# Kernel tuning notes

Measured on AMD Instinct MI355X. Metric: run time of the kernel, lower is better.

## Reference

```python
import jax, jax.numpy as jnp
import numpy as np

HEAD = 8


def setup_inputs() -> dict:
    key0 = jax.random.key(0)
    ks = jax.random.split(key0, 16)
    B, K, RD, NH = 16, 1024, 1024, 1024
    s = 0.02
    inp = {
        "v": jax.random.normal(ks[0], (B, K, RD), jnp.float32),
        "key": jax.random.normal(ks[1], (B, K, RD), jnp.float32),
        "query": jax.random.normal(ks[2], (B, K, RD), jnp.float32),
        "mask": jax.random.randint(ks[3], (B, 1, 1, K), 0, 2).astype(bool),
        # FCNet([relation_dim, num_hid], act='') == Linear(relation_dim, num_hid)
        "Wq": jax.random.normal(ks[4], (RD, NH), jnp.float32) * s,
        "bq": jnp.zeros((NH,), jnp.float32),
        "Wk": jax.random.normal(ks[5], (RD, NH), jnp.float32) * s,
        "bk": jnp.zeros((NH,), jnp.float32),
        "Wv": jax.random.normal(ks[6], (RD, NH), jnp.float32) * s,
        "bv": jnp.zeros((NH,), jnp.float32),
        "Wm": jax.random.normal(ks[7], (NH, NH), jnp.float32) * s,
        "bm": jnp.zeros((NH,), jnp.float32),
    }
    return inp


def reference(v, key, query, mask, Wq, bq, Wk, bk, Wv, bv, Wm, bm):
    B, K, _ = v.shape
    NH = Wq.shape[1]
    dk = NH // HEAD

    def split_heads(x):  # [B,K,NH] -> [B,H,K,dk]
        return x.reshape(B, K, HEAD, dk).transpose(0, 2, 1, 3)

    q = split_heads(query @ Wq + bq)
    k = split_heads(key @ Wk + bk)
    vv = split_heads(v @ Wv + bv)

    scores = jnp.einsum("bhqd,bhkd->bhqk", q, k) / jnp.sqrt(jnp.float32(dk))
    scores = jnp.where(mask, jnp.float32(-1e9), scores)
    att = jax.nn.softmax(scores, axis=-1)  # dropout is identity at eval
    atted = jnp.einsum("bhqk,bhkd->bhqd", att, vv)
    atted = atted.transpose(0, 2, 1, 3).reshape(B, K, NH)
    atted = atted @ Wm + bm
    return atted, att
```

## Files before the change

### kernel.cpp

```cpp
#include <hip/hip_runtime.h>

typedef unsigned short u16;
typedef __attribute__((ext_vector_type(8))) short short8;
typedef __attribute__((ext_vector_type(4))) float floatx4;

#define MFMA16(a, b, c) __builtin_amdgcn_mfma_f32_16x16x32_bf16(a, b, c, 0, 0, 0)

#define BB 16
#define KK 1024
#define NH 1024
#define HD 8
#define DK 128
#define ATT_OFF 16777216

typedef const __attribute__((address_space(1))) unsigned gl_u32;
typedef __attribute__((address_space(3))) unsigned lds_u32;

__device__ __forceinline__ u16 f2bf(float x) {
  unsigned u = __builtin_bit_cast(unsigned, x);
  u += 0x7fffu + ((u >> 16) & 1u);
  return (u16)(u >> 16);
}

__device__ __forceinline__ void gload16(const u16* g, u16* l) {
  __builtin_amdgcn_global_load_lds((gl_u32*)g, (lds_u32*)l, 16, 0, 0);
}

__global__ __launch_bounds__(256) void cast3_bf16x8(
    const float* __restrict__ i0, const float* __restrict__ i1,
    const float* __restrict__ i2, u16* __restrict__ o0, u16* __restrict__ o1,
    u16* __restrict__ o2) {
  const float* in = blockIdx.y == 0 ? i0 : (blockIdx.y == 1 ? i1 : i2);
  u16* out = blockIdx.y == 0 ? o0 : (blockIdx.y == 1 ? o1 : o2);
  const size_t i = ((size_t)blockIdx.x * 256 + threadIdx.x) * 8;
  float4 f0 = *(const float4*)(in + i);
  float4 f1 = *(const float4*)(in + i + 4);
  union { u16 u[8]; uint4 v; } p;
  p.u[0] = f2bf(f0.x); p.u[1] = f2bf(f0.y); p.u[2] = f2bf(f0.z); p.u[3] = f2bf(f0.w);
  p.u[4] = f2bf(f1.x); p.u[5] = f2bf(f1.y); p.u[6] = f2bf(f1.z); p.u[7] = f2bf(f1.w);
  *(uint4*)(out + i) = p.v;
}

__global__ __launch_bounds__(256) void tr_w(const float* __restrict__ in,
                                            u16* __restrict__ out) {
  __shared__ u16 t[32][36];
  const int tid = threadIdx.x;
  const int bx = blockIdx.x * 32;
  const int by = blockIdx.y * 32;
  const int r = tid >> 3, c4 = (tid & 7) * 4;
  float4 f = *(const float4*)(in + (size_t)(by + r) * 1024 + bx + c4);
  t[r][c4 + 0] = f2bf(f.x);
  t[r][c4 + 1] = f2bf(f.y);
  t[r][c4 + 2] = f2bf(f.z);
  t[r][c4 + 3] = f2bf(f.w);
  __syncthreads();
  union { u16 u[4]; uint2 v; } p;
#pragma unroll
  for (int i = 0; i < 4; i++) p.u[i] = t[c4 + i][r];
  *(uint2*)(out + (size_t)(bx + r) * 1024 + by + c4) = p.v;
}

__global__ __launch_bounds__(256) void tr_head(const u16* __restrict__ vvb,
                                               u16* __restrict__ vvT) {
  __shared__ u16 t[32][36];
  const int tid = threadIdx.x;
  const int bh = blockIdx.z, b = bh >> 3, h = bh & 7;
  const int i0 = blockIdx.x * 32, d0 = blockIdx.y * 32;
  const int r = tid >> 3, c4 = (tid & 7) * 4;
  union { u16 u[4]; uint2 v; } p;
  p.v = *(const uint2*)(vvb + (size_t)(b * KK + i0 + r) * NH + h * DK + d0 + c4);
  t[r][c4 + 0] = p.u[0];
  t[r][c4 + 1] = p.u[1];
  t[r][c4 + 2] = p.u[2];
  t[r][c4 + 3] = p.u[3];
  __syncthreads();
#pragma unroll
  for (int i = 0; i < 4; i++) p.u[i] = t[c4 + i][r];
  *(uint2*)(vvT + (size_t)(bh * DK + d0 + r) * KK + i0 + c4) = p.v;
}

__device__ __forceinline__ void gemm_body(
    const u16* __restrict__ Ab, const u16* __restrict__ Bb,
    const float* __restrict__ bias, u16* __restrict__ Cb, float* __restrict__ Cf,
    const int Kd, const int ldc, const int nBase, const int mBase) {
  __shared__ __align__(16) u16 As[2][128 * 32];
  __shared__ __align__(16) u16 Bs[2][128 * 32];
  const int tid = threadIdx.x;
  const int wid = tid >> 6, lane = tid & 63;
  const int wm = (wid & 1) * 64, wn = (wid >> 1) * 64;
  const int lm = lane & 15, lq = lane >> 4;
  const int rIn = lane >> 2;
  const int sSlot = (lane & 3) * 8;

  const u16* aS0 = Ab + (size_t)(mBase + (wid * 2 + 0) * 16 + rIn) * Kd + sSlot;
  const u16* aS1 = Ab + (size_t)(mBase + (wid * 2 + 1) * 16 + rIn) * Kd + sSlot;
  const u16* bS0 = Bb + (size_t)(nBase + (wid * 2 + 0) * 16 + rIn) * Kd + sSlot;
  const u16* bS1 = Bb + (size_t)(nBase + (wid * 2 + 1) * 16 + rIn) * Kd + sSlot;

  floatx4 acc[4][4] = {};

  gload16(aS0, &As[0][(wid * 2 + 0) * 512]);
  gload16(aS1, &As[0][(wid * 2 + 1) * 512]);
  gload16(bS0, &Bs[0][(wid * 2 + 0) * 512]);
  gload16(bS1, &Bs[0][(wid * 2 + 1) * 512]);
  __syncthreads();

  int cur = 0;
  for (int k0 = 0; k0 < Kd; k0 += 32) {
    const int nxt = cur ^ 1;
    if (k0 + 32 < Kd) {
      gload16(aS0 + k0 + 32, &As[nxt][(wid * 2 + 0) * 512]);
      gload16(aS1 + k0 + 32, &As[nxt][(wid * 2 + 1) * 512]);
      gload16(bS0 + k0 + 32, &Bs[nxt][(wid * 2 + 0) * 512]);
      gload16(bS1 + k0 + 32, &Bs[nxt][(wid * 2 + 1) * 512]);
    }
    short8 af[4], bfr[4];
#pragma unroll
    for (int t = 0; t < 4; t++) {
      af[t]  = *(const short8*)&As[cur][(wm + t * 16 + lm) * 32 + lq * 8];
      bfr[t] = *(const short8*)&Bs[cur][(wn + t * 16 + lm) * 32 + lq * 8];
    }
#pragma unroll
    for (int i = 0; i < 4; i++)
#pragma unroll
      for (int j = 0; j < 4; j++)
        acc[i][j] = MFMA16(af[i], bfr[j], acc[i][j]);
    __syncthreads();
    cur = nxt;
  }

#pragma unroll
  for (int i = 0; i < 4; i++) {
    const int rowL = wm + i * 16 + lq * 4;
#pragma unroll
    for (int j = 0; j < 4; j++) {
      const int col = nBase + wn + j * 16 + lm;
      const float bval = bias ? bias[col] : 0.0f;
      const size_t base = (size_t)(mBase + rowL) * ldc + col;
#pragma unroll
      for (int r = 0; r < 4; r++) {
        const float v = acc[i][j][r] + bval;
        if (Cb) Cb[base + (size_t)r * ldc] = f2bf(v);
        if (Cf) Cf[base + (size_t)r * ldc] = v;
      }
    }
  }
}

__device__ __forceinline__ int2 swz_grid() {
  const int flat = blockIdx.x + 8 * blockIdx.y;
  const int xcd = flat & 7, idx = flat >> 3;
  const int nflat = xcd * 128 + idx;
  return make_int2((nflat & 7) * 128, (nflat >> 3) * 128);
}

__global__ __launch_bounds__(256, 2) void gemm_bt(
    const u16* __restrict__ A, const u16* __restrict__ Bt,
    const float* __restrict__ bias, u16* __restrict__ Cb, float* __restrict__ Cf) {
  int2 nm = swz_grid();
  gemm_body(A, Bt, bias, Cb, Cf, 1024, 1024, nm.x, nm.y);
}

__global__ __launch_bounds__(256, 2) void gemm_qkv(
    const u16* __restrict__ A0, const u16* __restrict__ A1,
    const u16* __restrict__ A2, const u16* __restrict__ B0,
    const u16* __restrict__ B1, const u16* __restrict__ B2,
    const float* __restrict__ b0, const float* __restrict__ b1,
    const float* __restrict__ b2, u16* __restrict__ C0, u16* __restrict__ C1,
    u16* __restrict__ C2) {
  const int z = blockIdx.z;
  const u16* A = z == 0 ? A0 : (z == 1 ? A1 : A2);
  const u16* B = z == 0 ? B0 : (z == 1 ? B1 : B2);
  const float* bias = z == 0 ? b0 : (z == 1 ? b1 : b2);
  u16* C = z == 0 ? C0 : (z == 1 ? C1 : C2);
  int2 nm = swz_grid();
  gemm_body(A, B, bias, C, nullptr, 1024, 1024, nm.x, nm.y);
}

__global__ __launch_bounds__(256, 2) void scores_softmax_pv(
    const u16* __restrict__ qb, const u16* __restrict__ kb,
    const int* __restrict__ mask, const u16* __restrict__ vvT,
    float* __restrict__ att, u16* __restrict__ atp) {
  __shared__ __align__(16) u16 p_lds[16 * 1024];
  u16* msk16 = p_lds;
  float* redM = (float*)&p_lds[1024];
  float* redS = (float*)&p_lds[1152];
  const int tid = threadIdx.x;

  const int flat = blockIdx.x + 64 * blockIdx.y;
  const int xcd = flat & 7, idx = flat >> 3;
  const int bh = xcd * 16 + (idx >> 6);
  const int rowBlk = idx & 63;

  const int b = bh >> 3, h = bh & 7;
  const int wid = tid >> 6, lane = tid & 63;
  const int lm = lane & 15, lq = lane >> 4;
  const int rowG = rowBlk * 16;

  {
    int4 m = *(const int4*)(mask + (size_t)b * KK + tid * 4);
    msk16[tid * 4 + 0] = (u16)(m.x != 0);
    msk16[tid * 4 + 1] = (u16)(m.y != 0);
    msk16[tid * 4 + 2] = (u16)(m.z != 0);
    msk16[tid * 4 + 3] = (u16)(m.w != 0);
  }

  short8 qf[4];
  const u16* qp = qb + (size_t)(b * KK + rowG + lm) * NH + h * DK + lq * 8;
#pragma unroll
  for (int ks = 0; ks < 4; ks++) qf[ks] = *(const short8*)(qp + ks * 32);

  floatx4 acc[16] = {};
  const u16* kpB = kb + (size_t)(b * KK + wid * 256 + lm) * NH + h * DK + lq * 8;
  short8 kf[4][4];
#pragma unroll
  for (int p = 0; p < 4; p++) {
    const u16* kp = kpB + (size_t)p * 16 * NH;
    kf[p][0] = *(const short8*)(kp + 0);
    kf[p][1] = *(const short8*)(kp + 32);
    kf[p][2] = *(const short8*)(kp + 64);
    kf[p][3] = *(const short8*)(kp + 96);
  }
#pragma unroll
  for (int jt = 0; jt < 16; jt++) {
    const int slot = jt & 3;
    short8 c0 = kf[slot][0], c1 = kf[slot][1], c2 = kf[slot][2], c3 = kf[slot][3];
    if (jt + 4 < 16) {
      const u16* kp = kpB + (size_t)(jt + 4) * 16 * NH;
      kf[slot][0] = *(const short8*)(kp + 0);
      kf[slot][1] = *(const short8*)(kp + 32);
      kf[slot][2] = *(const short8*)(kp + 64);
      kf[slot][3] = *(const short8*)(kp + 96);
    }
    floatx4 a = acc[jt];
    a = MFMA16(qf[0], c0, a);
    a = MFMA16(qf[1], c1, a);
    a = MFMA16(qf[2], c2, a);
    a = MFMA16(qf[3], c3, a);
    acc[jt] = a;
  }
  __syncthreads();

  const float scale = 0.08838834764831845f;
  float mrow[4] = {-3e38f, -3e38f, -3e38f, -3e38f};
#pragma unroll
  for (int jt = 0; jt < 16; jt++) {
    const int col = wid * 256 + jt * 16 + lm;
    const bool mk = msk16[col] != 0;
#pragma unroll
    for (int r = 0; r < 4; r++) {
      float s = mk ? -1e9f : acc[jt][r] * scale;
      acc[jt][r] = s;
      mrow[r] = fmaxf(mrow[r], s);
    }
  }
#pragma unroll
  for (int off = 1; off < 16; off <<= 1)
#pragma unroll
    for (int r = 0; r < 4; r++) mrow[r] = fmaxf(mrow[r], __shfl_xor(mrow[r], off));
  if (lm == 0) {
#pragma unroll
    for (int r = 0; r < 4; r++) redM[wid * 16 + lq * 4 + r] = mrow[r];
  }
  __syncthreads();
#pragma unroll
  for (int r = 0; r < 4; r++)
    mrow[r] = fmaxf(fmaxf(redM[0 + lq * 4 + r], redM[16 + lq * 4 + r]),
                    fmaxf(redM[32 + lq * 4 + r], redM[48 + lq * 4 + r]));

  float srow[4] = {0.f, 0.f, 0.f, 0.f};
#pragma unroll
  for (int jt = 0; jt < 16; jt++)
#pragma unroll
    for (int r = 0; r < 4; r++) {
      float e = __expf(acc[jt][r] - mrow[r]);
      acc[jt][r] = e;
      srow[r] += e;
    }
#pragma unroll
  for (int off = 1; off < 16; off <<= 1)
#pragma unroll
    for (int r = 0; r < 4; r++) srow[r] += __shfl_xor(srow[r], off);
  if (lm == 0) {
#pragma unroll
    for (int r = 0; r < 4; r++) redS[wid * 16 + lq * 4 + r] = srow[r];
  }
  __syncthreads();
#pragma unroll
  for (int r = 0; r < 4; r++) {
    float s = redS[0 + lq * 4 + r] + redS[16 + lq * 4 + r] +
              redS[32 + lq * 4 + r] + redS[48 + lq * 4 + r];
    srow[r] = 1.0f / s;
  }
  __syncthreads();

#pragma unroll
  for (int r = 0; r < 4; r++) {
    const int row = lq * 4 + r;
    float* attRow = att + ((size_t)bh * KK + rowG + row) * KK;
#pragma unroll
    for (int jt = 0; jt < 16; jt++) {
      const int col = wid * 256 + jt * 16 + lm;
      const float p = acc[jt][r] * srow[r];
      __builtin_nontemporal_store(p, attRow + col);
      p_lds[(row * 1024 + col) ^ ((row & 7) << 3)] = f2bf(p);
    }
  }
  __syncthreads();

  floatx4 pacc0 = {}, pacc1 = {}, pacc2 = {}, pacc3 = {};
  const u16* vBase = vvT + (size_t)bh * DK * KK + (size_t)(wid * 32 + lm) * KK + lq * 8;
  short8 vf[4][2];
#pragma unroll
  for (int p = 0; p < 4; p++) {
    vf[p][0] = *(const short8*)(vBase + p * 32);
    vf[p][1] = *(const short8*)(vBase + 16 * KK + p * 32);
  }
#pragma unroll
  for (int s = 0; s < 32; s++) {
    const int slot = s & 3;
    short8 v0 = vf[slot][0], v1 = vf[slot][1];
    if (s + 4 < 32) {
      vf[slot][0] = *(const short8*)(vBase + (s + 4) * 32);
      vf[slot][1] = *(const short8*)(vBase + 16 * KK + (s + 4) * 32);
    }
    short8 pf = *(const short8*)&p_lds[(lm * 1024 + s * 32 + lq * 8) ^ ((lm & 7) << 3)];
    if (s & 1) {
      pacc2 = MFMA16(pf, v0, pacc2);
      pacc3 = MFMA16(pf, v1, pacc3);
    } else {
      pacc0 = MFMA16(pf, v0, pacc0);
      pacc1 = MFMA16(pf, v1, pacc1);
    }
  }
  floatx4 o0 = pacc0 + pacc2;
  floatx4 o1 = pacc1 + pacc3;

#pragma unroll
  for (int r = 0; r < 4; r++) {
    const int row = rowG + lq * 4 + r;
    atp[(size_t)(b * KK + row) * NH + h * DK + wid * 32 + 0 + lm] = f2bf(o0[r]);
    atp[(size_t)(b * KK + row) * NH + h * DK + wid * 32 + 16 + lm] = f2bf(o1[r]);
  }
}

extern "C" void kernel_launch(void* const* d_in, const int* in_sizes, int n_in,
                              void* d_out, int out_size, void* d_ws, size_t ws_size,
                              hipStream_t stream) {
  const float* v     = (const float*)d_in[0];
  const float* key   = (const float*)d_in[1];
  const float* query = (const float*)d_in[2];
  const int*   mask  = (const int*)d_in[3];
  const float* Wq = (const float*)d_in[4];
  const float* bq = (const float*)d_in[5];
  const float* Wk = (const float*)d_in[6];
  const float* bk = (const float*)d_in[7];
  const float* Wv = (const float*)d_in[8];
  const float* bv = (const float*)d_in[9];
  const float* Wm = (const float*)d_in[10];
  const float* bm = (const float*)d_in[11];

  float* atted = (float*)d_out;
  float* att   = atted + (size_t)ATT_OFF;

  char* ws = (char*)d_ws;
  u16* qb   = (u16*)(ws + 0);
  u16* kb   = (u16*)(ws + 33554432ll);
  u16* vvb  = (u16*)(ws + 67108864ll);
  u16* vvT  = (u16*)(ws + 100663296ll);
  u16* atp  = (u16*)(ws + 134217728ll);
  u16* WqT  = (u16*)(ws + 167772160ll);
  u16* WkT  = (u16*)(ws + 169869312ll);
  u16* WvT  = (u16*)(ws + 171966464ll);
  u16* WmT  = (u16*)(ws + 174063616ll);

  u16* cq = (u16*)att;
  u16* ck = cq + 16777216;
  u16* cv = ck + 16777216;

  cast3_bf16x8<<<dim3(8192, 3), 256, 0, stream>>>(query, key, v, cq, ck, cv);

  tr_w<<<dim3(32, 32), 256, 0, stream>>>(Wq, WqT);
  tr_w<<<dim3(32, 32), 256, 0, stream>>>(Wk, WkT);
  tr_w<<<dim3(32, 32), 256, 0, stream>>>(Wv, WvT);
  tr_w<<<dim3(32, 32), 256, 0, stream>>>(Wm, WmT);

  gemm_qkv<<<dim3(8, 128, 3), 256, 0, stream>>>(cq, ck, cv, WqT, WkT, WvT,
                                                bq, bk, bv, qb, kb, vvb);

  tr_head<<<dim3(32, 4, 128), 256, 0, stream>>>(vvb, vvT);

  scores_softmax_pv<<<dim3(64, 128), 256, 0, stream>>>(qb, kb, mask, vvT, att, atp);

  gemm_bt<<<dim3(8, 128), 256, 0, stream>>>(atp, WmT, bm, nullptr, atted);
}
```

Measured before the change: 1.329 ms.

## Process 32 query rows per attention block and merge weight transposes

The attention kernel now handles two 16-row query groups per block, so each K and V fragment loaded from global memory feeds two MFMA chains. This halves K/V reloads and block count. The explicit software prefetch of K and V is dropped, and the fp32 attention-probability stores are deferred until after the PV product. LDS doubles to 64KB and register pressure roughly doubles for the accumulators, which risks spills or lower occupancy under launch_bounds(256,2). The four weight-transpose launches are also merged into a single launch with a z-dimension.

```diff
diff --git a/kernel.cpp b/kernel.cpp
--- a/kernel.cpp
+++ b/kernel.cpp
@@ -41,8 +41,14 @@
   *(uint4*)(out + i) = p.v;
 }
 
-__global__ __launch_bounds__(256) void tr_w(const float* __restrict__ in,
-                                            u16* __restrict__ out) {
+__global__ __launch_bounds__(256) void tr_w4(
+    const float* __restrict__ w0, const float* __restrict__ w1,
+    const float* __restrict__ w2, const float* __restrict__ w3,
+    u16* __restrict__ o0, u16* __restrict__ o1, u16* __restrict__ o2,
+    u16* __restrict__ o3) {
+  const int z = blockIdx.z;
+  const float* in = z == 0 ? w0 : (z == 1 ? w1 : (z == 2 ? w2 : w3));
+  u16* out = z == 0 ? o0 : (z == 1 ? o1 : (z == 2 ? o2 : o3));
   __shared__ u16 t[32][36];
   const int tid = threadIdx.x;
   const int bx = blockIdx.x * 32;
@@ -181,21 +187,21 @@
     const u16* __restrict__ qb, const u16* __restrict__ kb,
     const int* __restrict__ mask, const u16* __restrict__ vvT,
     float* __restrict__ att, u16* __restrict__ atp) {
-  __shared__ __align__(16) u16 p_lds[16 * 1024];
+  __shared__ __align__(16) u16 p_lds[32 * 1024];
   u16* msk16 = p_lds;
   float* redM = (float*)&p_lds[1024];
-  float* redS = (float*)&p_lds[1152];
+  float* redS = (float*)&p_lds[1280];
   const int tid = threadIdx.x;
 
-  const int flat = blockIdx.x + 64 * blockIdx.y;
+  const int flat = blockIdx.x + 32 * blockIdx.y;
   const int xcd = flat & 7, idx = flat >> 3;
-  const int bh = xcd * 16 + (idx >> 6);
-  const int rowBlk = idx & 63;
+  const int bh = xcd * 16 + (idx >> 5);
+  const int rowBlk = idx & 31;
 
   const int b = bh >> 3, h = bh & 7;
   const int wid = tid >> 6, lane = tid & 63;
   const int lm = lane & 15, lq = lane >> 4;
-  const int rowG = rowBlk * 16;
+  const int rowG = rowBlk * 32;
 
   {
     int4 m = *(const int4*)(mask + (size_t)b * KK + tid * 4);
@@ -205,143 +211,164 @@
     msk16[tid * 4 + 3] = (u16)(m.w != 0);
   }
 
-  short8 qf[4];
-  const u16* qp = qb + (size_t)(b * KK + rowG + lm) * NH + h * DK + lq * 8;
-#pragma unroll
-  for (int ks = 0; ks < 4; ks++) qf[ks] = *(const short8*)(qp + ks * 32);
-
-  floatx4 acc[16] = {};
+  short8 qf[2][4];
+#pragma unroll
+  for (int g = 0; g < 2; g++) {
+    const u16* qp = qb + (size_t)(b * KK + rowG + g * 16 + lm) * NH + h * DK + lq * 8;
+#pragma unroll
+    for (int ks = 0; ks < 4; ks++) qf[g][ks] = *(const short8*)(qp + ks * 32);
+  }
+
+  floatx4 acc[2][16] = {};
   const u16* kpB = kb + (size_t)(b * KK + wid * 256 + lm) * NH + h * DK + lq * 8;
-  short8 kf[4][4];
-#pragma unroll
-  for (int p = 0; p < 4; p++) {
-    const u16* kp = kpB + (size_t)p * 16 * NH;
-    kf[p][0] = *(const short8*)(kp + 0);
-    kf[p][1] = *(const short8*)(kp + 32);
-    kf[p][2] = *(const short8*)(kp + 64);
-    kf[p][3] = *(const short8*)(kp + 96);
-  }
 #pragma unroll
   for (int jt = 0; jt < 16; jt++) {
-    const int slot = jt & 3;
-    short8 c0 = kf[slot][0], c1 = kf[slot][1], c2 = kf[slot][2], c3 = kf[slot][3];
-    if (jt + 4 < 16) {
-      const u16* kp = kpB + (size_t)(jt + 4) * 16 * NH;
-      kf[slot][0] = *(const short8*)(kp + 0);
-      kf[slot][1] = *(const short8*)(kp + 32);
-      kf[slot][2] = *(const short8*)(kp + 64);
-      kf[slot][3] = *(const short8*)(kp + 96);
-    }
-    floatx4 a = acc[jt];
-    a = MFMA16(qf[0], c0, a);
-    a = MFMA16(qf[1], c1, a);
-    a = MFMA16(qf[2], c2, a);
-    a = MFMA16(qf[3], c3, a);
-    acc[jt] = a;
+    const u16* kp = kpB + (size_t)jt * 16 * NH;
+    short8 k0 = *(const short8*)(kp + 0);
+    short8 k1 = *(const short8*)(kp + 32);
+    short8 k2 = *(const short8*)(kp + 64);
+    short8 k3 = *(const short8*)(kp + 96);
+    floatx4 a0 = acc[0][jt], a1 = acc[1][jt];
+    a0 = MFMA16(qf[0][0], k0, a0);
+    a1 = MFMA16(qf[1][0], k0, a1);
+    a0 = MFMA16(qf[0][1], k1, a0);
+    a1 = MFMA16(qf[1][1], k1, a1);
+    a0 = MFMA16(qf[0][2], k2, a0);
+    a1 = MFMA16(qf[1][2], k2, a1);
+    a0 = MFMA16(qf[0][3], k3, a0);
+    a1 = MFMA16(qf[1][3], k3, a1);
+    acc[0][jt] = a0;
+    acc[1][jt] = a1;
   }
   __syncthreads();
 
   const float scale = 0.08838834764831845f;
-  float mrow[4] = {-3e38f, -3e38f, -3e38f, -3e38f};
+  float mrow[2][4];
+#pragma unroll
+  for (int g = 0; g < 2; g++)
+#pragma unroll
+    for (int r = 0; r < 4; r++) mrow[g][r] = -3e38f;
 #pragma unroll
   for (int jt = 0; jt < 16; jt++) {
     const int col = wid * 256 + jt * 16 + lm;
     const bool mk = msk16[col] != 0;
 #pragma unroll
+    for (int g = 0; g < 2; g++)
+#pragma unroll
+      for (int r = 0; r < 4; r++) {
+        float s = mk ? -1e9f : acc[g][jt][r] * scale;
+        acc[g][jt][r] = s;
+        mrow[g][r] = fmaxf(mrow[g][r], s);
+      }
+  }
+#pragma unroll
+  for (int off = 1; off < 16; off <<= 1)
+#pragma unroll
+    for (int g = 0; g < 2; g++)
+#pragma unroll
+      for (int r = 0; r < 4; r++)
+        mrow[g][r] = fmaxf(mrow[g][r], __shfl_xor(mrow[g][r], off));
+  if (lm == 0) {
+#pragma unroll
+    for (int g = 0; g < 2; g++)
+#pragma unroll
+      for (int r = 0; r < 4; r++)
+        redM[wid * 32 + g * 16 + lq * 4 + r] = mrow[g][r];
+  }
+  __syncthreads();
+#pragma unroll
+  for (int g = 0; g < 2; g++)
+#pragma unroll
     for (int r = 0; r < 4; r++) {
-      float s = mk ? -1e9f : acc[jt][r] * scale;
-      acc[jt][r] = s;
-      mrow[r] = fmaxf(mrow[r], s);
-    }
-  }
+      const int e = g * 16 + lq * 4 + r;
+      mrow[g][r] = fmaxf(fmaxf(redM[0 + e], redM[32 + e]),
+                         fmaxf(redM[64 + e], redM[96 + e]));
+    }
+
+  float srow[2][4] = {};
+#pragma unroll
+  for (int jt = 0; jt < 16; jt++)
+#pragma unroll
+    for (int g = 0; g < 2; g++)
+#pragma unroll
+      for (int r = 0; r < 4; r++) {
+        float e = __expf(acc[g][jt][r] - mrow[g][r]);
+        acc[g][jt][r] = e;
+        srow[g][r] += e;
+      }
 #pragma unroll
   for (int off = 1; off < 16; off <<= 1)
 #pragma unroll
-    for (int r = 0; r < 4; r++) mrow[r] = fmaxf(mrow[r], __shfl_xor(mrow[r], off));
+    for (int g = 0; g < 2; g++)
+#pragma unroll
+      for (int r = 0; r < 4; r++) srow[g][r] += __shfl_xor(srow[g][r], off);
   if (lm == 0) {
 #pragma unroll
-    for (int r = 0; r < 4; r++) redM[wid * 16 + lq * 4 + r] = mrow[r];
-  }
-  __syncthreads();
-#pragma unroll
-  for (int r = 0; r < 4; r++)
-    mrow[r] = fmaxf(fmaxf(redM[0 + lq * 4 + r], redM[16 + lq * 4 + r]),
-                    fmaxf(redM[32 + lq * 4 + r], redM[48 + lq * 4 + r]));
-
-  float srow[4] = {0.f, 0.f, 0.f, 0.f};
-#pragma unroll
-  for (int jt = 0; jt < 16; jt++)
+    for (int g = 0; g < 2; g++)
+#pragma unroll
+      for (int r = 0; r < 4; r++)
+        redS[wid * 32 + g * 16 + lq * 4 + r] = srow[g][r];
+  }
+  __syncthreads();
+#pragma unroll
+  for (int g = 0; g < 2; g++)
 #pragma unroll
     for (int r = 0; r < 4; r++) {
-      float e = __expf(acc[jt][r] - mrow[r]);
-      acc[jt][r] = e;
-      srow[r] += e;
-    }
-#pragma unroll
-  for (int off = 1; off < 16; off <<= 1)
-#pragma unroll
-    for (int r = 0; r < 4; r++) srow[r] += __shfl_xor(srow[r], off);
-  if (lm == 0) {
-#pragma unroll
-    for (int r = 0; r < 4; r++) redS[wid * 16 + lq * 4 + r] = srow[r];
-  }
-  __syncthreads();
-#pragma unroll
-  for (int r = 0; r < 4; r++) {
-    float s = redS[0 + lq * 4 + r] + redS[16 + lq * 4 + r] +
-              redS[32 + lq * 4 + r] + redS[48 + lq * 4 + r];
-    srow[r] = 1.0f / s;
-  }
-  __syncthreads();
-
-#pragma unroll
-  for (int r = 0; r < 4; r++) {
-    const int row = lq * 4 + r;
-    float* attRow = att + ((size_t)bh * KK + rowG + row) * KK;
-#pragma unroll
-    for (int jt = 0; jt < 16; jt++) {
-      const int col = wid * 256 + jt * 16 + lm;
-      const float p = acc[jt][r] * srow[r];
-      __builtin_nontemporal_store(p, attRow + col);
-      p_lds[(row * 1024 + col) ^ ((row & 7) << 3)] = f2bf(p);
-    }
-  }
-  __syncthreads();
-
-  floatx4 pacc0 = {}, pacc1 = {}, pacc2 = {}, pacc3 = {};
+      const int e = g * 16 + lq * 4 + r;
+      srow[g][r] = 1.0f / (redS[0 + e] + redS[32 + e] + redS[64 + e] + redS[96 + e]);
+    }
+  __syncthreads();
+
+#pragma unroll
+  for (int g = 0; g < 2; g++)
+#pragma unroll
+    for (int r = 0; r < 4; r++) {
+      const int row = g * 16 + lq * 4 + r;
+#pragma unroll
+      for (int jt = 0; jt < 16; jt++) {
+        const int col = wid * 256 + jt * 16 + lm;
+        const float p = acc[g][jt][r] * srow[g][r];
+        acc[g][jt][r] = p;
+        p_lds[(row * 1024 + col) ^ ((row & 7) << 3)] = f2bf(p);
+      }
+    }
+  __syncthreads();
+
+  floatx4 pacc[2][2] = {};
   const u16* vBase = vvT + (size_t)bh * DK * KK + (size_t)(wid * 32 + lm) * KK + lq * 8;
-  short8 vf[4][2];
-#pragma unroll
-  for (int p = 0; p < 4; p++) {
-    vf[p][0] = *(const short8*)(vBase + p * 32);
-    vf[p][1] = *(const short8*)(vBase + 16 * KK + p * 32);
-  }
-#pragma unroll
+#pragma unroll 8
   for (int s = 0; s < 32; s++) {
-    const int slot = s & 3;
-    short8 v0 = vf[slot][0], v1 = vf[slot][1];
-    if (s + 4 < 32) {
-      vf[slot][0] = *(const short8*)(vBase + (s + 4) * 32);
-      vf[slot][1] = *(const short8*)(vBase + 16 * KK + (s + 4) * 32);
-    }
-    short8 pf = *(const short8*)&p_lds[(lm * 1024 + s * 32 + lq * 8) ^ ((lm & 7) << 3)];
-    if (s & 1) {
-      pacc2 = MFMA16(pf, v0, pacc2);
-      pacc3 = MFMA16(pf, v1, pacc3);
-    } else {
-      pacc0 = MFMA16(pf, v0, pacc0);
-      pacc1 = MFMA16(pf, v1, pacc1);
-    }
-  }
-  floatx4 o0 = pacc0 + pacc2;
-  floatx4 o1 = pacc1 + pacc3;
-
-#pragma unroll
-  for (int r = 0; r < 4; r++) {
-    const int row = rowG + lq * 4 + r;
-    atp[(size_t)(b * KK + row) * NH + h * DK + wid * 32 + 0 + lm] = f2bf(o0[r]);
-    atp[(size_t)(b * KK + row) * NH + h * DK + wid * 32 + 16 + lm] = f2bf(o1[r]);
-  }
+    short8 v0 = *(const short8*)(vBase + s * 32);
+    short8 v1 = *(const short8*)(vBase + 16 * KK + s * 32);
+    short8 pf0 = *(const short8*)&p_lds[((0 + lm) * 1024 + s * 32 + lq * 8) ^ ((lm & 7) << 3)];
+    short8 pf1 = *(const short8*)&p_lds[((16 + lm) * 1024 + s * 32 + lq * 8) ^ ((lm & 7) << 3)];
+    pacc[0][0] = MFMA16(pf0, v0, pacc[0][0]);
+    pacc[0][1] = MFMA16(pf0, v1, pacc[0][1]);
+    pacc[1][0] = MFMA16(pf1, v0, pacc[1][0]);
+    pacc[1][1] = MFMA16(pf1, v1, pacc[1][1]);
+  }
+
+#pragma unroll
+  for (int g = 0; g < 2; g++)
+#pragma unroll
+    for (int r = 0; r < 4; r++) {
+      const int row = rowG + g * 16 + lq * 4 + r;
+      atp[(size_t)(b * KK + row) * NH + h * DK + wid * 32 + 0 + lm] = f2bf(pacc[g][0][r]);
+      atp[(size_t)(b * KK + row) * NH + h * DK + wid * 32 + 16 + lm] = f2bf(pacc[g][1][r]);
+    }
+
+#pragma unroll
+  for (int g = 0; g < 2; g++)
+#pragma unroll
+    for (int r = 0; r < 4; r++) {
+      const int row = g * 16 + lq * 4 + r;
+      float* attRow = att + ((size_t)bh * KK + rowG + row) * KK;
+#pragma unroll
+      for (int jt = 0; jt < 16; jt++) {
+        const int col = wid * 256 + jt * 16 + lm;
+        __builtin_nontemporal_store(acc[g][jt][r], attRow + col);
+      }
+    }
 }
 
 extern "C" void kernel_launch(void* const* d_in, const int* in_sizes, int n_in,
@@ -380,17 +407,14 @@
 
   cast3_bf16x8<<<dim3(8192, 3), 256, 0, stream>>>(query, key, v, cq, ck, cv);
 
-  tr_w<<<dim3(32, 32), 256, 0, stream>>>(Wq, WqT);
-  tr_w<<<dim3(32, 32), 256, 0, stream>>>(Wk, WkT);
-  tr_w<<<dim3(32, 32), 256, 0, stream>>>(Wv, WvT);
-  tr_w<<<dim3(32, 32), 256, 0, stream>>>(Wm, WmT);
+  tr_w4<<<dim3(32, 32, 4), 256, 0, stream>>>(Wq, Wk, Wv, Wm, WqT, WkT, WvT, WmT);
 
   gemm_qkv<<<dim3(8, 128, 3), 256, 0, stream>>>(cq, ck, cv, WqT, WkT, WvT,
                                                 bq, bk, bv, qb, kb, vvb);
 
   tr_head<<<dim3(32, 4, 128), 256, 0, stream>>>(vvb, vvT);
 
-  scores_softmax_pv<<<dim3(64, 128), 256, 0, stream>>>(qb, kb, mask, vvT, att, atp);
+  scores_softmax_pv<<<dim3(32, 128), 256, 0, stream>>>(qb, kb, mask, vvT, att, atp);
 
   gemm_bt<<<dim3(8, 128), 256, 0, stream>>>(atp, WmT, bm, nullptr, atted);
 }
```

Result: faster. 1.122 ms (-15.6%).
